# Kernel optimization log

Measured on AMD Instinct MI355X. Metric: run time of the kernel, lower is better.

The kernel has to match this reference:

```python
import jax, jax.numpy as jnp
import numpy as np

D_MODEL = 1024
NUM_HEADS = 16
DEPTH = D_MODEL // NUM_HEADS


def setup_inputs() -> dict:
    key = jax.random.key(0)
    ks = jax.random.split(key, 11)
    B, S = 2, 2048
    s = 1.0 / np.sqrt(D_MODEL)
    return {
        "q": jax.random.normal(ks[0], (B, S, D_MODEL), jnp.float32),
        "k": jax.random.normal(ks[1], (B, S, D_MODEL), jnp.float32),
        "v": jax.random.normal(ks[2], (B, S, D_MODEL), jnp.float32),
        "wq": jax.random.normal(ks[3], (D_MODEL, D_MODEL), jnp.float32) * s,
        "bq": jax.random.normal(ks[4], (D_MODEL,), jnp.float32) * s,
        "wk": jax.random.normal(ks[5], (D_MODEL, D_MODEL), jnp.float32) * s,
        "bk": jax.random.normal(ks[6], (D_MODEL,), jnp.float32) * s,
        "wv": jax.random.normal(ks[7], (D_MODEL, D_MODEL), jnp.float32) * s,
        "bv": jax.random.normal(ks[8], (D_MODEL,), jnp.float32) * s,
        "wo": jax.random.normal(ks[9], (D_MODEL, D_MODEL), jnp.float32) * s,
        "bo": jax.random.normal(ks[10], (D_MODEL,), jnp.float32) * s,
    }


def _split_heads(x, B):
    # [B, S, D] -> [B, H, S, depth]
    return x.reshape(B, -1, NUM_HEADS, DEPTH).transpose(0, 2, 1, 3)


def reference(q, k, v, wq, bq, wk, bk, wv, bv, wo, bo):
    B, S, _ = q.shape
    # torch Linear: y = x @ W.T + b
    qh = _split_heads(q @ wq.T + bq, B)
    kh = _split_heads(k @ wk.T + bk, B)
    vh = _split_heads(v @ wv.T + bv, B)
    scale = jnp.sqrt(jnp.asarray(DEPTH, jnp.float32))
    scores = jnp.einsum("bhqd,bhkd->bhqk", qh, kh) / scale  # [B,H,S,S]
    attn = jax.nn.softmax(scores, axis=-1)
    out = jnp.einsum("bhqk,bhkd->bhqd", attn, vh)
    out = out.transpose(0, 2, 1, 3).reshape(B, S, D_MODEL)
    return out @ wo.T + bo
```

## Files before the change

### kernel.cpp

```cpp
#include <hip/hip_runtime.h>
#include <hip/hip_bf16.h>
#include <math.h>

#define D_MODEL 1024
#define NUM_HEADS 16
#define DEPTH 64
#define BATCH 2
#define SEQ 2048
#define N_TOK (BATCH * SEQ)

typedef short bf16x8 __attribute__((ext_vector_type(8)));
typedef _Float16 f16x8 __attribute__((ext_vector_type(8)));
typedef float f32x4  __attribute__((ext_vector_type(4)));
typedef unsigned short u16x8 __attribute__((ext_vector_type(8)));
typedef unsigned short u16x4 __attribute__((ext_vector_type(4)));

__device__ __forceinline__ unsigned short f2b(float x) {
    return __builtin_bit_cast(unsigned short, __float2bfloat16(x));
}
__device__ __forceinline__ float b2f(unsigned short h) {
    return __builtin_bit_cast(float, (unsigned int)h << 16);
}
__device__ __forceinline__ unsigned short f2h(float x) {
    return __builtin_bit_cast(unsigned short, (_Float16)x);
}

__global__ __launch_bounds__(256) void split_f16(
    const float* __restrict__ src,
    unsigned short* __restrict__ dst,
    int n8)
{
    const int i = blockIdx.x * 256 + threadIdx.x;
    if (i >= n8) return;
    const float4 f0 = ((const float4*)src)[2 * i];
    const float4 f1 = ((const float4*)src)[2 * i + 1];
    const float xs[8] = {f0.x, f0.y, f0.z, f0.w, f1.x, f1.y, f1.z, f1.w};
    u16x8 o;
    #pragma unroll
    for (int e = 0; e < 8; ++e) o[e] = f2h(xs[e]);
    *(u16x8*)&dst[(size_t)i * 8] = o;
}

__global__ __launch_bounds__(256) void prep_weights(
    const float* __restrict__ s0, const float* __restrict__ s1,
    const float* __restrict__ s2, const float* __restrict__ s3,
    unsigned short* __restrict__ f0, unsigned short* __restrict__ f1,
    unsigned short* __restrict__ f2,
    unsigned short* __restrict__ h3, unsigned short* __restrict__ l3,
    int n8)
{
    const int i = blockIdx.x * 256 + threadIdx.x;
    if (i >= n8) return;
    const int which = blockIdx.y;
    const float* src = (which == 0) ? s0 : (which == 1) ? s1 : (which == 2) ? s2 : s3;
    const float4 a0 = ((const float4*)src)[2 * i];
    const float4 a1 = ((const float4*)src)[2 * i + 1];
    const float xs[8] = {a0.x, a0.y, a0.z, a0.w, a1.x, a1.y, a1.z, a1.w};
    if (which < 3) {
        unsigned short* dst = (which == 0) ? f0 : (which == 1) ? f1 : f2;
        u16x8 o;
        #pragma unroll
        for (int e = 0; e < 8; ++e) o[e] = f2h(xs[e]);
        *(u16x8*)&dst[(size_t)i * 8] = o;
    } else {
        u16x8 h8, l8;
        #pragma unroll
        for (int e = 0; e < 8; ++e) {
            const unsigned short h = f2b(xs[e]);
            h8[e] = h;
            l8[e] = f2b(xs[e] - b2f(h));
        }
        *(u16x8*)&h3[(size_t)i * 8] = h8;
        *(u16x8*)&l3[(size_t)i * 8] = l8;
    }
}

__global__ __launch_bounds__(256, 4) void gemm_f16(
    const unsigned short* __restrict__ Af,
    const unsigned short* __restrict__ Bf,
    const float* __restrict__ bias,
    void* __restrict__ Yv,
    float scale,
    int mode)
{
    __shared__ unsigned short sA[64][64];
    __shared__ unsigned short sB[64][64];

    const int tid  = threadIdx.x;
    const int wave = tid >> 6;
    const int lane = tid & 63;
    const int quad = lane >> 4;
    const int l16  = lane & 15;
    const int wm   = wave >> 1;
    const int wn   = wave & 1;

    const int j0 = blockIdx.x * 64;
    const int i0 = blockIdx.y * 64;

    const int sc  = tid & 7;
    const int r32 = tid >> 3;

    u16x8 pre[4];
    #pragma unroll
    for (int p = 0; p < 4; ++p) {
        const bool isA = p < 2;
        const int row = (p & 1) * 32 + r32;
        const unsigned short* src = isA ? Af : Bf;
        const int grow = (isA ? i0 : j0) + row;
        const int cg = (sc ^ (row & 7)) * 8;
        pre[p] = *(const u16x8*)&src[(size_t)grow * 1024 + cg];
    }

    f32x4 acc[2][2] = {};

    for (int s = 0; s < 16; ++s) {
        __syncthreads();

        #pragma unroll
        for (int p = 0; p < 4; ++p) {
            const bool isA = p < 2;
            const int row = (p & 1) * 32 + r32;
            unsigned short (*dst)[64] = isA ? sA : sB;
            *(u16x8*)&dst[row][sc * 8] = pre[p];
        }
        __syncthreads();

        if (s + 1 < 16) {
            const int k0 = (s + 1) * 64;
            #pragma unroll
            for (int p = 0; p < 4; ++p) {
                const bool isA = p < 2;
                const int row = (p & 1) * 32 + r32;
                const unsigned short* src = isA ? Af : Bf;
                const int grow = (isA ? i0 : j0) + row;
                const int cg = (sc ^ (row & 7)) * 8;
                pre[p] = *(const u16x8*)&src[(size_t)grow * 1024 + k0 + cg];
            }
        }

        #pragma unroll
        for (int ks = 0; ks < 2; ++ks) {
            f16x8 a[2], b[2];
            #pragma unroll
            for (int mt = 0; mt < 2; ++mt) {
                const int row = wm * 32 + mt * 16 + l16;
                const int c = (((ks * 4 + quad) ^ (row & 7))) * 8;
                a[mt] = *(const f16x8*)&sA[row][c];
            }
            #pragma unroll
            for (int nt = 0; nt < 2; ++nt) {
                const int row = wn * 32 + nt * 16 + l16;
                const int c = (((ks * 4 + quad) ^ (row & 7))) * 8;
                b[nt] = *(const f16x8*)&sB[row][c];
            }
            #pragma unroll
            for (int mt = 0; mt < 2; ++mt)
                #pragma unroll
                for (int nt = 0; nt < 2; ++nt)
                    acc[mt][nt] = __builtin_amdgcn_mfma_f32_16x16x32_f16(a[mt], b[nt], acc[mt][nt], 0, 0, 0);
        }
    }

    float bv[2];
    #pragma unroll
    for (int nt = 0; nt < 2; ++nt)
        bv[nt] = bias[j0 + wn * 32 + nt * 16 + l16];

    #pragma unroll
    for (int mt = 0; mt < 2; ++mt) {
        const int ibase = i0 + wm * 32 + mt * 16 + quad * 4;
        #pragma unroll
        for (int nt = 0; nt < 2; ++nt) {
            const int j = j0 + wn * 32 + nt * 16 + l16;
            const int h = j >> 6, d = j & 63;
            if (mode == 1) {
                __hip_bfloat16* Y = (__hip_bfloat16*)Yv;
                #pragma unroll
                for (int r = 0; r < 4; ++r) {
                    const int i = ibase + r;
                    const int b = i >> 11, ss = i & (SEQ - 1);
                    Y[(((size_t)(b * NUM_HEADS + h) * SEQ) + ss) * DEPTH + d] =
                        __float2bfloat16((acc[mt][nt][r] + bv[nt]) * scale);
                }
            } else {
                unsigned short* Y = (unsigned short*)Yv;
                const int b = ibase >> 11;
                u16x4 pack;
                #pragma unroll
                for (int r = 0; r < 4; ++r)
                    pack[r] = f2b((acc[mt][nt][r] + bv[nt]) * scale);
                *(u16x4*)&Y[(((size_t)(b * NUM_HEADS + h) * DEPTH) + d) * SEQ
                            + (ibase & (SEQ - 1))] = pack;
            }
        }
    }
}

__global__ __launch_bounds__(512, 2) void gemm_bf16x3(
    const unsigned short* __restrict__ Ahi,
    const unsigned short* __restrict__ Alo,
    const unsigned short* __restrict__ Bhi,
    const unsigned short* __restrict__ Blo,
    const float* __restrict__ bias,
    float* __restrict__ Y,
    float scale)
{
    __shared__ unsigned short sAh[128][64];
    __shared__ unsigned short sAl[128][64];
    __shared__ unsigned short sBh[128][64];
    __shared__ unsigned short sBl[128][64];

    const int tid  = threadIdx.x;
    const int wave = tid >> 6;
    const int lane = tid & 63;
    const int quad = lane >> 4;
    const int l16  = lane & 15;
    const int wm   = wave >> 1;
    const int wn   = wave & 1;

    const int j0 = blockIdx.x * 128;
    const int i0 = blockIdx.y * 128;

    const int sc  = tid & 7;
    const int r64 = tid >> 3;

    u16x8 preH[4], preL[4];

    #pragma unroll
    for (int p = 0; p < 4; ++p) {
        const int row256 = p * 64 + r64;
        const bool isA = row256 < 128;
        const int row = isA ? row256 : row256 - 128;
        const unsigned short* srcH = isA ? Ahi : Bhi;
        const unsigned short* srcL = isA ? Alo : Blo;
        const int grow = (isA ? i0 : j0) + row;
        const int cg = (sc ^ (row & 7)) * 8;
        const size_t go = (size_t)grow * 1024 + cg;
        preH[p] = *(const u16x8*)&srcH[go];
        preL[p] = *(const u16x8*)&srcL[go];
    }

    f32x4 acc[2][4] = {};

    for (int s = 0; s < 16; ++s) {
        __syncthreads();

        #pragma unroll
        for (int p = 0; p < 4; ++p) {
            const int row256 = p * 64 + r64;
            const bool isA = row256 < 128;
            const int row = isA ? row256 : row256 - 128;
            unsigned short (*dh)[64] = isA ? sAh : sBh;
            unsigned short (*dl)[64] = isA ? sAl : sBl;
            *(u16x8*)&dh[row][sc * 8] = preH[p];
            *(u16x8*)&dl[row][sc * 8] = preL[p];
        }
        __syncthreads();

        if (s + 1 < 16) {
            const int k0 = (s + 1) * 64;
            #pragma unroll
            for (int p = 0; p < 4; ++p) {
                const int row256 = p * 64 + r64;
                const bool isA = row256 < 128;
                const int row = isA ? row256 : row256 - 128;
                const unsigned short* srcH = isA ? Ahi : Bhi;
                const unsigned short* srcL = isA ? Alo : Blo;
                const int grow = (isA ? i0 : j0) + row;
                const int cg = (sc ^ (row & 7)) * 8;
                const size_t go = (size_t)grow * 1024 + k0 + cg;
                preH[p] = *(const u16x8*)&srcH[go];
                preL[p] = *(const u16x8*)&srcL[go];
            }
        }

        #pragma unroll
        for (int ks = 0; ks < 2; ++ks) {
            bf16x8 ah[2], al[2], bh[4], bl[4];
            #pragma unroll
            for (int mt = 0; mt < 2; ++mt) {
                const int row = wm * 32 + mt * 16 + l16;
                const int c = (((ks * 4 + quad) ^ (row & 7))) * 8;
                ah[mt] = *(const bf16x8*)&sAh[row][c];
                al[mt] = *(const bf16x8*)&sAl[row][c];
            }
            #pragma unroll
            for (int nt = 0; nt < 4; ++nt) {
                const int row = wn * 64 + nt * 16 + l16;
                const int c = (((ks * 4 + quad) ^ (row & 7))) * 8;
                bh[nt] = *(const bf16x8*)&sBh[row][c];
                bl[nt] = *(const bf16x8*)&sBl[row][c];
            }
            #pragma unroll
            for (int mt = 0; mt < 2; ++mt)
                #pragma unroll
                for (int nt = 0; nt < 4; ++nt) {
                    acc[mt][nt] = __builtin_amdgcn_mfma_f32_16x16x32_bf16(ah[mt], bh[nt], acc[mt][nt], 0, 0, 0);
                    acc[mt][nt] = __builtin_amdgcn_mfma_f32_16x16x32_bf16(ah[mt], bl[nt], acc[mt][nt], 0, 0, 0);
                    acc[mt][nt] = __builtin_amdgcn_mfma_f32_16x16x32_bf16(al[mt], bh[nt], acc[mt][nt], 0, 0, 0);
                }
        }
    }

    float bv[4];
    #pragma unroll
    for (int nt = 0; nt < 4; ++nt)
        bv[nt] = bias[j0 + wn * 64 + nt * 16 + l16];

    #pragma unroll
    for (int mt = 0; mt < 2; ++mt) {
        const int ibase = i0 + wm * 32 + mt * 16 + quad * 4;
        #pragma unroll
        for (int nt = 0; nt < 4; ++nt) {
            const int j = j0 + wn * 64 + nt * 16 + l16;
            #pragma unroll
            for (int r = 0; r < 4; ++r)
                Y[(size_t)(ibase + r) * 1024 + j] = (acc[mt][nt][r] + bv[nt]) * scale;
        }
    }
}

__global__ __launch_bounds__(256) void flash_attn_mfma(
    const __hip_bfloat16* __restrict__ Qg,
    const __hip_bfloat16* __restrict__ Kg,
    const __hip_bfloat16* __restrict__ Vg,
    unsigned short* __restrict__ OHi,
    unsigned short* __restrict__ OLo)
{
    __shared__ unsigned short Ks[64][72];
    __shared__ unsigned short Vt[64][72];
    __shared__ unsigned short Ps[4][16][68];

    const int tid  = threadIdx.x;
    const int wave = tid >> 6;
    const int lane = tid & 63;
    const int quad = lane >> 4;
    const int l16  = lane & 15;

    const int bh = blockIdx.x >> 5;
    const int q0 = (blockIdx.x & 31) * 64;

    const unsigned short* Qu = (const unsigned short*)Qg + (size_t)bh * SEQ * DEPTH;
    const unsigned short* Ku = (const unsigned short*)Kg + (size_t)bh * SEQ * DEPTH;
    const unsigned short* Vu = (const unsigned short*)Vg + (size_t)bh * DEPTH * SEQ;

    const int qrow = q0 + wave * 16 + l16;
    bf16x8 qf[2];
    qf[0] = *(const bf16x8*)&Qu[(size_t)qrow * DEPTH + quad * 8];
    qf[1] = *(const bf16x8*)&Qu[(size_t)qrow * DEPTH + 32 + quad * 8];

    bf16x8 ones;
    #pragma unroll
    for (int e = 0; e < 8; ++e) ones[e] = (short)0x3F80;

    f32x4 o_acc[4] = {};
    f32x4 l_acc = {0.f, 0.f, 0.f, 0.f};

    const int srow = tid >> 3;
    const int sc8  = (tid & 7) * 8;
    u16x8 kpre[2], vpre[2];
    #pragma unroll
    for (int it = 0; it < 2; ++it) {
        const int row = it * 32 + srow;
        kpre[it] = *(const u16x8*)&Ku[(size_t)row * DEPTH + sc8];
        vpre[it] = *(const u16x8*)&Vu[(size_t)row * SEQ + sc8];
    }

    for (int t = 0; t < 32; ++t) {
        __syncthreads();

        #pragma unroll
        for (int it = 0; it < 2; ++it) {
            const int row = it * 32 + srow;
            *(u16x8*)&Ks[row][sc8] = kpre[it];
            *(u16x8*)&Vt[row][sc8] = vpre[it];
        }
        __syncthreads();

        if (t + 1 < 32) {
            const int k0 = (t + 1) * 64;
            #pragma unroll
            for (int it = 0; it < 2; ++it) {
                const int row = it * 32 + srow;
                kpre[it] = *(const u16x8*)&Ku[(size_t)(k0 + row) * DEPTH + sc8];
                vpre[it] = *(const u16x8*)&Vu[(size_t)row * SEQ + k0 + sc8];
            }
        }

        f32x4 s[4];
        #pragma unroll
        for (int nt = 0; nt < 4; ++nt) {
            s[nt] = f32x4{0.f, 0.f, 0.f, 0.f};
            bf16x8 kf0 = *(const bf16x8*)&Ks[nt * 16 + l16][quad * 8];
            s[nt] = __builtin_amdgcn_mfma_f32_16x16x32_bf16(qf[0], kf0, s[nt], 0, 0, 0);
            bf16x8 kf1 = *(const bf16x8*)&Ks[nt * 16 + l16][32 + quad * 8];
            s[nt] = __builtin_amdgcn_mfma_f32_16x16x32_bf16(qf[1], kf1, s[nt], 0, 0, 0);
        }

        #pragma unroll
        for (int nt = 0; nt < 4; ++nt)
            #pragma unroll
            for (int r = 0; r < 4; ++r)
                Ps[wave][quad * 4 + r][nt * 16 + l16] = f2b(__expf(s[nt][r]));

        __builtin_amdgcn_wave_barrier();
        __asm__ volatile("s_waitcnt lgkmcnt(0)" ::: "memory");
        __builtin_amdgcn_wave_barrier();

        bf16x8 pf[2];
        {
            u16x4 a0 = *(const u16x4*)&Ps[wave][l16][quad * 8];
            u16x4 a1 = *(const u16x4*)&Ps[wave][l16][quad * 8 + 4];
            u16x4 b0 = *(const u16x4*)&Ps[wave][l16][32 + quad * 8];
            u16x4 b1 = *(const u16x4*)&Ps[wave][l16][32 + quad * 8 + 4];
            #pragma unroll
            for (int e = 0; e < 4; ++e) {
                pf[0][e] = (short)a0[e]; pf[0][4 + e] = (short)a1[e];
                pf[1][e] = (short)b0[e]; pf[1][4 + e] = (short)b1[e];
            }
        }

        #pragma unroll
        for (int nt = 0; nt < 4; ++nt) {
            bf16x8 vf0 = *(const bf16x8*)&Vt[nt * 16 + l16][quad * 8];
            o_acc[nt] = __builtin_amdgcn_mfma_f32_16x16x32_bf16(pf[0], vf0, o_acc[nt], 0, 0, 0);
            bf16x8 vf1 = *(const bf16x8*)&Vt[nt * 16 + l16][32 + quad * 8];
            o_acc[nt] = __builtin_amdgcn_mfma_f32_16x16x32_bf16(pf[1], vf1, o_acc[nt], 0, 0, 0);
        }
        l_acc = __builtin_amdgcn_mfma_f32_16x16x32_bf16(pf[0], ones, l_acc, 0, 0, 0);
        l_acc = __builtin_amdgcn_mfma_f32_16x16x32_bf16(pf[1], ones, l_acc, 0, 0, 0);
    }

    const int b = bh / NUM_HEADS;
    const int h = bh % NUM_HEADS;
    #pragma unroll
    for (int r = 0; r < 4; ++r) {
        const float inv = 1.f / l_acc[r];
        const int row = q0 + wave * 16 + quad * 4 + r;
        #pragma unroll
        for (int nt = 0; nt < 4; ++nt) {
            const float o = o_acc[nt][r] * inv;
            const size_t idx = ((size_t)(b * SEQ + row)) * D_MODEL + h * DEPTH + nt * 16 + l16;
            const unsigned short hbits = f2b(o);
            OHi[idx] = hbits;
            OLo[idx] = f2b(o - b2f(hbits));
        }
    }
}

extern "C" void kernel_launch(void* const* d_in, const int* in_sizes, int n_in,
                              void* d_out, int out_size, void* d_ws, size_t ws_size,
                              hipStream_t stream) {
    const float* q  = (const float*)d_in[0];
    const float* k  = (const float*)d_in[1];
    const float* v  = (const float*)d_in[2];
    const float* wq = (const float*)d_in[3];
    const float* bq = (const float*)d_in[4];
    const float* wk = (const float*)d_in[5];
    const float* bk = (const float*)d_in[6];
    const float* wv = (const float*)d_in[7];
    const float* bv = (const float*)d_in[8];
    const float* wo = (const float*)d_in[9];
    const float* bo = (const float*)d_in[10];
    float* out = (float*)d_out;

    char* ws = (char*)d_ws;
    const size_t MB = 1024 * 1024;
    unsigned short* Af16 = (unsigned short*)(ws);
    unsigned short* AoHi = (unsigned short*)(ws);
    unsigned short* AoLo = (unsigned short*)(ws + 8 * MB);
    unsigned short* WqF  = (unsigned short*)(ws + 16 * MB);
    unsigned short* WkF  = (unsigned short*)(ws + 18 * MB);
    unsigned short* WvF  = (unsigned short*)(ws + 20 * MB);
    unsigned short* WoH  = (unsigned short*)(ws + 22 * MB);
    unsigned short* WoL  = (unsigned short*)(ws + 24 * MB);
    __hip_bfloat16* Qh   = (__hip_bfloat16*)(ws + 26 * MB);
    __hip_bfloat16* Kh   = (__hip_bfloat16*)(ws + 34 * MB);
    __hip_bfloat16* Vh   = (__hip_bfloat16*)(ws + 42 * MB);

    const int nW8 = D_MODEL * D_MODEL / 8;
    const int nA8 = N_TOK * D_MODEL / 8;
    dim3 sb(256);

    prep_weights<<<dim3(nW8 / 256, 4), sb, 0, stream>>>(
        wq, wk, wv, wo, WqF, WkF, WvF, WoH, WoL, nW8);

    dim3 fblk(256);
    dim3 fgrid(D_MODEL / 64, N_TOK / 64);

    split_f16<<<dim3(nA8 / 256), sb, 0, stream>>>(q, Af16, nA8);
    gemm_f16<<<fgrid, fblk, 0, stream>>>(Af16, WqF, bq, Qh, 0.125f, 1);
    split_f16<<<dim3(nA8 / 256), sb, 0, stream>>>(k, Af16, nA8);
    gemm_f16<<<fgrid, fblk, 0, stream>>>(Af16, WkF, bk, Kh, 1.0f, 1);
    split_f16<<<dim3(nA8 / 256), sb, 0, stream>>>(v, Af16, nA8);
    gemm_f16<<<fgrid, fblk, 0, stream>>>(Af16, WvF, bv, Vh, 1.0f, 2);

    dim3 ablk(256);
    dim3 agrid(BATCH * NUM_HEADS * (SEQ / 64));
    flash_attn_mfma<<<agrid, ablk, 0, stream>>>(Qh, Kh, Vh, AoHi, AoLo);

    dim3 oblk(512);
    dim3 ogrid(D_MODEL / 128, N_TOK / 128);
    gemm_bf16x3<<<ogrid, oblk, 0, stream>>>(AoHi, AoLo, WoH, WoL, bo, out, 1.0f);
}
```

Measured before the change: 274.5 us.

## Double-buffer GEMM LDS tiles with direct global-to-LDS async loads

Replaces the register-staged prefetch in the f16 projection GEMM with global_load_lds, which writes 16-byte chunks straight from global memory into one of two LDS buffers. The next k-tile loads into the idle buffer while MFMAs run on the current one, with one barrier per iteration instead of two. This removes the register round trip and a sync per step, but doubles LDS use per block (16KB), which may lower occupancy. It also depends on the builtin placing each lane's 16-byte chunk at the intended per-lane LDS address.

```diff
diff --git a/kernel.cpp b/kernel.cpp
--- a/kernel.cpp
+++ b/kernel.cpp
@@ -83,8 +83,8 @@
     float scale,
     int mode)
 {
-    __shared__ unsigned short sA[64][64];
-    __shared__ unsigned short sB[64][64];
+    __shared__ unsigned short sA[2][64][64];
+    __shared__ unsigned short sB[2][64][64];
 
     const int tid  = threadIdx.x;
     const int wave = tid >> 6;
@@ -100,43 +100,33 @@
     const int sc  = tid & 7;
     const int r32 = tid >> 3;
 
-    u16x8 pre[4];
-    #pragma unroll
-    for (int p = 0; p < 4; ++p) {
-        const bool isA = p < 2;
-        const int row = (p & 1) * 32 + r32;
-        const unsigned short* src = isA ? Af : Bf;
-        const int grow = (isA ? i0 : j0) + row;
-        const int cg = (sc ^ (row & 7)) * 8;
-        pre[p] = *(const u16x8*)&src[(size_t)grow * 1024 + cg];
-    }
-
     f32x4 acc[2][2] = {};
 
-    for (int s = 0; s < 16; ++s) {
-        __syncthreads();
-
+    auto stage = [&](int buf, int s) {
+        const int k0 = s * 64;
         #pragma unroll
         for (int p = 0; p < 4; ++p) {
             const bool isA = p < 2;
             const int row = (p & 1) * 32 + r32;
-            unsigned short (*dst)[64] = isA ? sA : sB;
-            *(u16x8*)&dst[row][sc * 8] = pre[p];
-        }
-        __syncthreads();
-
-        if (s + 1 < 16) {
-            const int k0 = (s + 1) * 64;
-            #pragma unroll
-            for (int p = 0; p < 4; ++p) {
-                const bool isA = p < 2;
-                const int row = (p & 1) * 32 + r32;
-                const unsigned short* src = isA ? Af : Bf;
-                const int grow = (isA ? i0 : j0) + row;
-                const int cg = (sc ^ (row & 7)) * 8;
-                pre[p] = *(const u16x8*)&src[(size_t)grow * 1024 + k0 + cg];
-            }
-        }
+            const unsigned short* src = isA ? Af : Bf;
+            const int grow = (isA ? i0 : j0) + row;
+            const int cg = (sc ^ (row & 7)) * 8;
+            unsigned short (*dst)[64] = isA ? sA[buf] : sB[buf];
+            __builtin_amdgcn_global_load_lds(
+                (const __attribute__((address_space(1))) unsigned int*)
+                    &src[(size_t)grow * 1024 + k0 + cg],
+                (__attribute__((address_space(3))) unsigned int*)&dst[row][sc * 8],
+                16, 0, 0);
+        }
+    };
+
+    stage(0, 0);
+    __asm__ volatile("s_waitcnt vmcnt(0)" ::: "memory");
+    __syncthreads();
+
+    int cur = 0;
+    for (int s = 0; s < 16; ++s) {
+        if (s + 1 < 16) stage(cur ^ 1, s + 1);
 
         #pragma unroll
         for (int ks = 0; ks < 2; ++ks) {
@@ -145,13 +135,13 @@
             for (int mt = 0; mt < 2; ++mt) {
                 const int row = wm * 32 + mt * 16 + l16;
                 const int c = (((ks * 4 + quad) ^ (row & 7))) * 8;
-                a[mt] = *(const f16x8*)&sA[row][c];
+                a[mt] = *(const f16x8*)&sA[cur][row][c];
             }
             #pragma unroll
             for (int nt = 0; nt < 2; ++nt) {
                 const int row = wn * 32 + nt * 16 + l16;
                 const int c = (((ks * 4 + quad) ^ (row & 7))) * 8;
-                b[nt] = *(const f16x8*)&sB[row][c];
+                b[nt] = *(const f16x8*)&sB[cur][row][c];
             }
             #pragma unroll
             for (int mt = 0; mt < 2; ++mt)
@@ -159,6 +149,10 @@
                 for (int nt = 0; nt < 2; ++nt)
                     acc[mt][nt] = __builtin_amdgcn_mfma_f32_16x16x32_f16(a[mt], b[nt], acc[mt][nt], 0, 0, 0);
         }
+
+        __asm__ volatile("s_waitcnt vmcnt(0)" ::: "memory");
+        __syncthreads();
+        cur ^= 1;
     }
 
     float bv[2];
```

After: 272.6 us. Within noise of the previous version (-0.7%).
